# Optimization experiments

Hardware: AMD Instinct MI355X
Metric: run time of the kernel (lower is better)

## Reference

```python
import jax, jax.numpy as jnp
import numpy as np

STRIDE = 1  # stride3x3 init arg


def sparsemax(z):
    """Sparsemax along last axis (Martins & Astudillo 2016)."""
    K = z.shape[-1]
    zs = -jnp.sort(-z, axis=-1)                     # sorted descending
    cum = jnp.cumsum(zs, axis=-1)
    ks = jnp.arange(1, K + 1, dtype=z.dtype)
    support = (1 + ks * zs) > cum                   # [.., K] bool
    k_z = jnp.sum(support, axis=-1, keepdims=True)  # support size, int
    cum_k = jnp.take_along_axis(cum, k_z - 1, axis=-1)
    tau = (cum_k - 1) / k_z.astype(z.dtype)
    return jnp.maximum(z - tau, 0)


def setup_inputs() -> dict:
    key = jax.random.key(0)
    k1, k2, k3, k4 = jax.random.split(key, 4)
    B, Cin, Cout, H, W, K = 64, 512, 512, 28, 28, 8
    x = jax.random.normal(k1, (B, Cin, H, W), dtype=jnp.float32)
    gate_w = jax.random.normal(k2, (K, Cin), dtype=jnp.float32) * 0.02   # nn.Linear weight
    gate_b = jax.random.normal(k3, (K,), dtype=jnp.float32) * 0.02       # nn.Linear bias
    expert_w = jax.random.normal(k4, (K, Cout, Cin), dtype=jnp.float32) * 0.02  # K conv1x1 kernels (bias-free)
    return {"x": x, "gate_w": gate_w, "gate_b": gate_b, "expert_w": expert_w}


def reference(x, gate_w, gate_b, expert_w):
    # gate: sparsemax(Linear(mean_pool(x)))
    pooled = x.mean(axis=(2, 3))                         # [B, Cin]
    g = sparsemax(pooled @ gate_w.T + gate_b)            # [B, K], many exact zeros
    # sum_k g[b,k] * conv1x1_k(x) == conv1x1 with per-sample combined weight
    xs = x[:, :, ::STRIDE, ::STRIDE]                     # 1x1 conv with stride = subsample
    w_eff = jnp.einsum('bk,koi->boi', g, expert_w)       # [B, Cout, Cin]
    out = jnp.einsum('boi,bihw->bohw', w_eff, xs)        # [B, Cout, H', W']
    return out
```

## Files before the change

### kernel.cpp

```cpp
#include <hip/hip_runtime.h>

#define NB 64
#define CIN 512
#define COUT 512
#define HW 784
#define KEXP 8

typedef __attribute__((ext_vector_type(8))) short bf16x8;
typedef __attribute__((ext_vector_type(4))) float f32x4;

typedef const __attribute__((address_space(1))) unsigned int GU32;
typedef __attribute__((address_space(3))) unsigned int LU32;

__device__ __forceinline__ unsigned f2bf1(float f) {
  unsigned u = __builtin_bit_cast(unsigned, f);
  return (u + 0x7FFFu + ((u >> 16) & 1u)) >> 16;
}
__device__ __forceinline__ unsigned f2bf2(float lo, float hi) {
  return f2bf1(lo) | (f2bf1(hi) << 16);
}

__global__ __launch_bounds__(256) void xtpool_kernel(const float* __restrict__ x,
                                                     uint4* __restrict__ xt,
                                                     float* __restrict__ parts) {
  __shared__ float tile[32][113];
  int id = blockIdx.x;
  int kk = id & 15, bn = id >> 4;
  int b = bn / 7, nb = bn - b * 7;
  const float* xsrc = x + (size_t)b * (CIN * HW) + (size_t)kk * 32 * HW + nb * 112;
  uint4* dst = xt + (size_t)id * 448;
  int t = threadIdx.x;

  #pragma unroll
  for (int i = 0; i < 14; ++i) {
    int idx = t + i * 256;
    int r = idx / 112, cc = idx - r * 112;
    tile[r][cc] = xsrc[(size_t)r * HW + cc];
  }
  __syncthreads();

  {
    int pr = t >> 3, pp = t & 7;
    float s = 0.f;
    #pragma unroll
    for (int i = 0; i < 14; ++i) s += tile[pr][pp * 14 + i];
    s += __shfl_xor(s, 1); s += __shfl_xor(s, 2); s += __shfl_xor(s, 4);
    if (pp == 0) parts[((size_t)nb * NB + b) * CIN + kk * 32 + pr] = s;
  }

  {
    int k0 = t / 112, c0 = t - k0 * 112;
    uint4 pk;
    pk.x = f2bf2(tile[k0 * 8 + 0][c0], tile[k0 * 8 + 1][c0]);
    pk.y = f2bf2(tile[k0 * 8 + 2][c0], tile[k0 * 8 + 3][c0]);
    pk.z = f2bf2(tile[k0 * 8 + 4][c0], tile[k0 * 8 + 5][c0]);
    pk.w = f2bf2(tile[k0 * 8 + 6][c0], tile[k0 * 8 + 7][c0]);
    dst[t] = pk;
  }
  if (t < 192) {
    int t2 = 256 + t, k1 = t2 / 112, c1 = t2 - k1 * 112;
    uint4 pk;
    pk.x = f2bf2(tile[k1 * 8 + 0][c1], tile[k1 * 8 + 1][c1]);
    pk.y = f2bf2(tile[k1 * 8 + 2][c1], tile[k1 * 8 + 3][c1]);
    pk.z = f2bf2(tile[k1 * 8 + 4][c1], tile[k1 * 8 + 5][c1]);
    pk.w = f2bf2(tile[k1 * 8 + 6][c1], tile[k1 * 8 + 7][c1]);
    dst[256 + t] = pk;
  }
}

__global__ __launch_bounds__(256) void gate_kernel(const float* __restrict__ parts,
                                                   const float* __restrict__ gw,
                                                   const float* __restrict__ gb,
                                                   float* __restrict__ g) {
  __shared__ float red[4][KEXP];
  int b = blockIdx.x;
  int t = threadIdx.x;
  int lane = t & 63, w = t >> 6;

  float p0 = 0.f, p1 = 0.f;
  #pragma unroll
  for (int q = 0; q < 7; ++q) {
    const float* pr = parts + (size_t)q * (NB * CIN) + b * CIN;
    p0 += pr[t];
    p1 += pr[t + 256];
  }
  float zk[KEXP];
  #pragma unroll
  for (int k = 0; k < KEXP; ++k)
    zk[k] = p0 * gw[k * CIN + t] + p1 * gw[k * CIN + t + 256];

  #pragma unroll
  for (int k = 0; k < KEXP; ++k) {
    float s = zk[k];
    #pragma unroll
    for (int off = 32; off; off >>= 1) s += __shfl_down(s, off);
    if (lane == 0) red[w][k] = s;
  }
  __syncthreads();

  if (t == 0) {
    float z[8], zs[8];
    #pragma unroll
    for (int j = 0; j < 8; ++j) {
      z[j] = (red[0][j] + red[1][j] + red[2][j] + red[3][j]) * (1.0f / 784.0f) + gb[j];
      zs[j] = z[j];
    }
    #pragma unroll
    for (int a = 1; a < 8; ++a) {
      float v = zs[a]; int j = a;
      while (j > 0 && zs[j - 1] < v) { zs[j] = zs[j - 1]; --j; }
      zs[j] = v;
    }
    float cums[8]; float csum = 0.f;
    #pragma unroll
    for (int j = 0; j < 8; ++j) { csum += zs[j]; cums[j] = csum; }
    int kz = 0;
    #pragma unroll
    for (int j = 0; j < 8; ++j)
      if (1.0f + (float)(j + 1) * zs[j] > cums[j]) kz = j + 1;
    float tau = (cums[kz - 1] - 1.0f) / (float)kz;
    #pragma unroll
    for (int j = 0; j < 8; ++j) g[b * 8 + j] = fmaxf(z[j] - tau, 0.0f);
  }
}

__global__ __launch_bounds__(256) void weff_kernel(const float* __restrict__ E,
                                                   const float* __restrict__ g,
                                                   uint4* __restrict__ wt) {
  __shared__ float gs[NB * KEXP];
  int t = threadIdx.x;
  ((float2*)gs)[t] = ((const float2*)g)[t];
  int o = blockIdx.x * 16 + (t & 15);
  int i = blockIdx.y * 128 + (t >> 4) * 8;
  int b0 = blockIdx.z * 32;
  float e[8][8];
  #pragma unroll
  for (int k = 0; k < 8; ++k) {
    const float4* p = (const float4*)(E + (size_t)k * (COUT * CIN) + (size_t)o * CIN + i);
    float4 a = p[0], c = p[1];
    e[k][0] = a.x; e[k][1] = a.y; e[k][2] = a.z; e[k][3] = a.w;
    e[k][4] = c.x; e[k][5] = c.y; e[k][6] = c.z; e[k][7] = c.w;
  }
  __syncthreads();
  int base = ((o >> 8) * 16 + (i >> 5)) * 1024 + ((i >> 3) & 3) * 256 + (o & 255);
  for (int b = b0; b < b0 + 32; ++b) {
    float acc[8] = {0, 0, 0, 0, 0, 0, 0, 0};
    #pragma unroll
    for (int k = 0; k < 8; ++k) {
      float gv = gs[b * 8 + k];
      #pragma unroll
      for (int j = 0; j < 8; ++j) acc[j] += gv * e[k][j];
    }
    uint4 pk;
    pk.x = f2bf2(acc[0], acc[1]); pk.y = f2bf2(acc[2], acc[3]);
    pk.z = f2bf2(acc[4], acc[5]); pk.w = f2bf2(acc[6], acc[7]);
    wt[(size_t)base + (size_t)b * 32768] = pk;
  }
}

#define VMCNT(n) asm volatile("s_waitcnt vmcnt(" #n ")" ::: "memory")
__global__ __launch_bounds__(512) void gemm_kernel(const uint4* __restrict__ weff,
                                                   const uint4* __restrict__ xt,
                                                   float* __restrict__ out) {
  __shared__ uint4 ldsA[3][1024];
  __shared__ uint4 ldsB[3][448];
  int id = blockIdx.x;
  int xcd = id & 7, s = id >> 3;
  int bloc = s / 14, inner = s - bloc * 14;
  int b = xcd * 8 + bloc;
  int mb = inner & 1, nb = inner >> 1;

  int t = threadIdx.x;
  int lane = t & 63, w = t >> 6;
  int l15 = lane & 15, l4 = lane >> 4;

  const uint4* asrc = weff + (size_t)b * 32768 + (size_t)mb * 16384;
  const uint4* bsrc = xt + (size_t)(b * 7 + nb) * 7168;

  int s1 = w * 64 + lane, fs1 = s1 ^ ((s1 >> 3) & 7);

  f32x4 acc[2][7] = {};

#define STAGE(buf, kk)                                                          \
  do {                                                                          \
    _Pragma("unroll")                                                           \
    for (int it = 0; it < 2; ++it)                                              \
      __builtin_amdgcn_global_load_lds((GU32*)(asrc + (kk) * 1024 + it * 512 + t), \
                                       (LU32*)(&ldsA[buf][it * 512 + w * 64]), 16, 0, 0); \
    if (w < 7)                                                                  \
      __builtin_amdgcn_global_load_lds((GU32*)(bsrc + (kk) * 448 + fs1),        \
                                       (LU32*)(&ldsB[buf][w * 64]), 16, 0, 0);  \
  } while (0)

  STAGE(0, 0);
  STAGE(1, 1);

  int cur = 0;
  for (int kk = 0; kk < 16; ++kk) {
    if (kk < 15) {
      if (w < 7) VMCNT(3); else VMCNT(2);
    } else {
      VMCNT(0);
    }
    __builtin_amdgcn_s_barrier();
    __builtin_amdgcn_sched_barrier(0);

    if (kk < 14) {
      int nxt = cur + 2; if (nxt >= 3) nxt -= 3;
      STAGE(nxt, kk + 2);
    }

    bf16x8 af[2];
    #pragma unroll
    for (int m = 0; m < 2; ++m)
      af[m] = *(const bf16x8*)&ldsA[cur][l4 * 256 + w * 32 + m * 16 + l15];
    #pragma unroll
    for (int u = 0; u < 7; ++u) {
      int un = l4 * 112 + u * 16 + l15;
      bf16x8 bf = *(const bf16x8*)&ldsB[cur][un ^ ((un >> 3) & 7)];
      #pragma unroll
      for (int m = 0; m < 2; ++m)
        acc[m][u] = __builtin_amdgcn_mfma_f32_16x16x32_bf16(af[m], bf, acc[m][u], 0, 0, 0);
    }

    if (++cur >= 3) cur = 0;
  }
#undef STAGE

  int orow0 = mb * 256 + w * 32 + l4 * 4;
  int col = nb * 112 + l15;
  #pragma unroll
  for (int m = 0; m < 2; ++m) {
    #pragma unroll
    for (int u = 0; u < 7; ++u) {
      float* op = out + ((size_t)b * COUT + orow0 + m * 16) * HW + col + u * 16;
      #pragma unroll
      for (int r = 0; r < 4; ++r) op[(size_t)r * HW] = acc[m][u][r];
    }
  }
}

extern "C" void kernel_launch(void* const* d_in, const int* in_sizes, int n_in,
                              void* d_out, int out_size, void* d_ws, size_t ws_size,
                              hipStream_t stream) {
  const float* x        = (const float*)d_in[0];
  const float* gate_w   = (const float*)d_in[1];
  const float* gate_b   = (const float*)d_in[2];
  const float* expert_w = (const float*)d_in[3];
  float* out = (float*)d_out;

  char* ws = (char*)d_ws;
  uint4* weff   = (uint4*)ws;
  uint4* xt     = (uint4*)(ws + 33554432);
  float* parts  = (float*)(ws + 33554432 + 51380224);
  float* g      = (float*)(ws + 33554432 + 51380224 + 917504);

  xtpool_kernel<<<7168, 256, 0, stream>>>(x, xt, parts);
  gate_kernel<<<NB, 256, 0, stream>>>(parts, gate_w, gate_b, g);
  weff_kernel<<<dim3(32, 4, 2), 256, 0, stream>>>(expert_w, g, weff);
  gemm_kernel<<<896, 512, 0, stream>>>(weff, xt, out);
}
```

Measured before the change: 90.86 us.

## Load GEMM A fragments directly into registers instead of staging through LDS

In the GEMM kernel, each wave's A operand (per-sample combined weights) is now fetched with inline global_load_dwordx4 straight into a double-buffered register set, instead of going through a triple-buffered LDS tile. This works because each wave reads only its own rows of A, so the LDS staging gave no sharing. Removing it cuts LDS capacity and LDS read/write traffic. Only the B tile still goes through LDS. The loop is fully unrolled, and the refill is moved after the MFMAs, using vmcnt waits tied to the register buffers. This relies on fragile inline-asm ordering that the compiler cannot see.

```diff
diff --git a/kernel.cpp b/kernel.cpp
--- a/kernel.cpp
+++ b/kernel.cpp
@@ -8,6 +8,7 @@
 
 typedef __attribute__((ext_vector_type(8))) short bf16x8;
 typedef __attribute__((ext_vector_type(4))) float f32x4;
+typedef __attribute__((ext_vector_type(4))) unsigned int u32x4;
 
 typedef const __attribute__((address_space(1))) unsigned int GU32;
 typedef __attribute__((address_space(3))) unsigned int LU32;
@@ -158,11 +159,9 @@
   }
 }
 
-#define VMCNT(n) asm volatile("s_waitcnt vmcnt(" #n ")" ::: "memory")
 __global__ __launch_bounds__(512) void gemm_kernel(const uint4* __restrict__ weff,
                                                    const uint4* __restrict__ xt,
                                                    float* __restrict__ out) {
-  __shared__ uint4 ldsA[3][1024];
   __shared__ uint4 ldsB[3][448];
   int id = blockIdx.x;
   int xcd = id & 7, s = id >> 3;
@@ -174,58 +173,59 @@
   int lane = t & 63, w = t >> 6;
   int l15 = lane & 15, l4 = lane >> 4;
 
-  const uint4* asrc = weff + (size_t)b * 32768 + (size_t)mb * 16384;
+  const uint4* asrc = weff + (size_t)b * 32768 + (size_t)mb * 16384
+                      + l4 * 256 + w * 32 + l15;
   const uint4* bsrc = xt + (size_t)(b * 7 + nb) * 7168;
 
   int s1 = w * 64 + lane, fs1 = s1 ^ ((s1 >> 3) & 7);
 
   f32x4 acc[2][7] = {};
-
-#define STAGE(buf, kk)                                                          \
-  do {                                                                          \
-    _Pragma("unroll")                                                           \
-    for (int it = 0; it < 2; ++it)                                              \
-      __builtin_amdgcn_global_load_lds((GU32*)(asrc + (kk) * 1024 + it * 512 + t), \
-                                       (LU32*)(&ldsA[buf][it * 512 + w * 64]), 16, 0, 0); \
-    if (w < 7)                                                                  \
-      __builtin_amdgcn_global_load_lds((GU32*)(bsrc + (kk) * 448 + fs1),        \
-                                       (LU32*)(&ldsB[buf][w * 64]), 16, 0, 0);  \
+  u32x4 a[2][2];
+
+#define LOADA(dst, kk, m)                                                     \
+  asm volatile("global_load_dwordx4 %0, %1, off"                              \
+               : "=v"(dst) : "v"((const void*)(asrc + (kk) * 1024 + (m) * 16)))
+#define STAGEB(kk)                                                            \
+  do { if (w < 7)                                                             \
+    __builtin_amdgcn_global_load_lds((GU32*)(bsrc + (kk) * 448 + fs1),        \
+                                     (LU32*)(&ldsB[(kk) % 3][s1]), 16, 0, 0); \
   } while (0)
-
-  STAGE(0, 0);
-  STAGE(1, 1);
-
-  int cur = 0;
+#define WAITTILE(n, x, y)                                                     \
+  asm volatile("s_waitcnt vmcnt(" #n ")" : "+v"(x), "+v"(y) :: "memory")
+
+  STAGEB(0); LOADA(a[0][0], 0, 0); LOADA(a[0][1], 0, 1);
+  STAGEB(1); LOADA(a[1][0], 1, 0); LOADA(a[1][1], 1, 1);
+
+  #pragma unroll
   for (int kk = 0; kk < 16; ++kk) {
     if (kk < 15) {
-      if (w < 7) VMCNT(3); else VMCNT(2);
+      if (w < 7) { WAITTILE(3, a[kk & 1][0], a[kk & 1][1]); }
+      else       { WAITTILE(2, a[kk & 1][0], a[kk & 1][1]); }
     } else {
-      VMCNT(0);
+      WAITTILE(0, a[kk & 1][0], a[kk & 1][1]);
     }
     __builtin_amdgcn_s_barrier();
     __builtin_amdgcn_sched_barrier(0);
 
-    if (kk < 14) {
-      int nxt = cur + 2; if (nxt >= 3) nxt -= 3;
-      STAGE(nxt, kk + 2);
-    }
-
-    bf16x8 af[2];
-    #pragma unroll
-    for (int m = 0; m < 2; ++m)
-      af[m] = *(const bf16x8*)&ldsA[cur][l4 * 256 + w * 32 + m * 16 + l15];
+    bf16x8 af0 = __builtin_bit_cast(bf16x8, a[kk & 1][0]);
+    bf16x8 af1 = __builtin_bit_cast(bf16x8, a[kk & 1][1]);
     #pragma unroll
     for (int u = 0; u < 7; ++u) {
       int un = l4 * 112 + u * 16 + l15;
-      bf16x8 bf = *(const bf16x8*)&ldsB[cur][un ^ ((un >> 3) & 7)];
-      #pragma unroll
-      for (int m = 0; m < 2; ++m)
-        acc[m][u] = __builtin_amdgcn_mfma_f32_16x16x32_bf16(af[m], bf, acc[m][u], 0, 0, 0);
-    }
-
-    if (++cur >= 3) cur = 0;
-  }
-#undef STAGE
+      bf16x8 bf = *(const bf16x8*)&ldsB[kk % 3][un ^ ((un >> 3) & 7)];
+      acc[0][u] = __builtin_amdgcn_mfma_f32_16x16x32_bf16(af0, bf, acc[0][u], 0, 0, 0);
+      acc[1][u] = __builtin_amdgcn_mfma_f32_16x16x32_bf16(af1, bf, acc[1][u], 0, 0, 0);
+    }
+
+    if (kk < 14) {
+      STAGEB(kk + 2);
+      LOADA(a[kk & 1][0], kk + 2, 0);
+      LOADA(a[kk & 1][1], kk + 2, 1);
+    }
+  }
+#undef LOADA
+#undef STAGEB
+#undef WAITTILE
 
   int orow0 = mb * 256 + w * 32 + l4 * 4;
   int col = nb * 112 + l15;
```

New measurement: 92.71 us. +2.0%, slower.
